# Kernel optimization log

Measured on AMD Instinct MI355X. Metric: run time of the kernel, lower is better.

Reference implementation:

```python
import jax, jax.numpy as jnp
import numpy as np

B, N, DIN, DOUT = 4, 4096, 128, 64
SCALE = float(DOUT)  # scale defaults to out_features


def setup_inputs() -> dict:
    key = jax.random.key(0)
    kx, kq, kk, kv = jax.random.split(key, 4)
    x = jax.random.normal(kx, (B, N, DIN), dtype=jnp.float32)
    # nn.Linear weights, stored as [in, out] so projection is x @ W
    Wq = jax.random.normal(kq, (DIN, DOUT), dtype=jnp.float32) * 0.02
    Wk = jax.random.normal(kk, (DIN, DOUT), dtype=jnp.float32) * 0.02
    Wv = jax.random.normal(kv, (DIN, DOUT), dtype=jnp.float32) * 0.02
    return {"x": x, "Wq": Wq, "Wk": Wk, "Wv": Wv}


def reference(x, Wq, Wk, Wv):
    # Projections: [B, N, DOUT]
    q = jnp.einsum("bnd,de->bne", x, Wq)
    k = jnp.einsum("bnd,de->bne", x, Wk)
    v = jnp.einsum("bnd,de->bne", x, Wv)
    # torch.cdist(q, k, p=2): Euclidean distance matrix [B, N, N]
    q_sq = jnp.sum(q * q, axis=-1)  # [B, N]
    k_sq = jnp.sum(k * k, axis=-1)  # [B, N]
    d2 = q_sq[:, :, None] + k_sq[:, None, :] - 2.0 * jnp.einsum("bne,bme->bnm", q, k)
    dist = jnp.sqrt(jnp.maximum(d2, 0.0))  # clamp for numerical safety
    att = jax.nn.softmax(dist / jnp.sqrt(jnp.float32(SCALE)), axis=-1)
    return jnp.einsum("bnm,bme->bne", att, v)
```

## Files before the change

kernel.cpp:

```cpp
#include <hip/hip_runtime.h>
#include <cstdint>
#include <cstddef>

#define B_ 4
#define N_ 4096
#define DIN_ 128

#define C2_ 0.0325213905f
#define NEG2C2_ (-0.0650427810f)

typedef __attribute__((ext_vector_type(8))) short short8;
typedef __attribute__((ext_vector_type(4))) float f32x4;
typedef __attribute__((ext_vector_type(4))) unsigned short us4;
typedef __attribute__((ext_vector_type(4))) unsigned int u32x4;

#if defined(__has_builtin)
#if __has_builtin(__builtin_amdgcn_exp2f)
#define EXP2(x) __builtin_amdgcn_exp2f(x)
#else
#define EXP2(x) exp2f(x)
#endif
#else
#define EXP2(x) exp2f(x)
#endif

__device__ __forceinline__ unsigned short f2bf(float f) {
    union { float f; unsigned int i; } v; v.f = f;
    unsigned int i = v.i;
    return (unsigned short)((i + 0x7FFFu + ((i >> 16) & 1u)) >> 16);
}

__device__ __forceinline__ unsigned int cvt_pk_bf16(float lo, float hi) {
    unsigned int r;
    asm("v_cvt_pk_bf16_f32 %0, %1, %2" : "=v"(r) : "v"(lo), "v"(hi));
    return r;
}

__global__ __launch_bounds__(256, 2) void proj_kernel(
    const float* __restrict__ x, const float* __restrict__ Wq,
    const float* __restrict__ Wk, const float* __restrict__ Wv,
    unsigned short* __restrict__ qb, unsigned short* __restrict__ kb,
    unsigned short* __restrict__ vT, float* __restrict__ qsq,
    float* __restrict__ ksq)
{
    __shared__ float xl[64 * 132];
    __shared__ float wl[128 * 64];
    const int t = threadIdx.x;
    const int R0 = blockIdx.x * 64;
    const int proj = blockIdx.y;
    const float* __restrict__ W = (proj == 0) ? Wq : ((proj == 1) ? Wk : Wv);

#pragma unroll
    for (int j = 0; j < 8; ++j) {
        const int i = t + 256 * j;
        const int row = i >> 5, dc = i & 31;
        *(float4*)(&xl[row * 132 + dc * 4]) =
            *(const float4*)(x + (size_t)(R0 + row) * DIN_ + dc * 4);
    }
#pragma unroll
    for (int j = 0; j < 8; ++j) {
        const int i = t + 256 * j;
        *(float4*)(&wl[i * 4]) = *(const float4*)(W + (size_t)i * 4);
    }
    __syncthreads();

    const int cg = t & 15, rg = t >> 4;
    const int c0 = cg * 4, r0 = rg * 4;

    float acc[4][4];
#pragma unroll
    for (int r = 0; r < 4; ++r)
#pragma unroll
        for (int c = 0; c < 4; ++c) acc[r][c] = 0.f;

    for (int d4 = 0; d4 < 32; ++d4) {
        float4 xv[4];
#pragma unroll
        for (int r = 0; r < 4; ++r)
            xv[r] = *(const float4*)(&xl[(r0 + r) * 132 + d4 * 4]);
#pragma unroll
        for (int dd = 0; dd < 4; ++dd) {
            const float4 wv = *(const float4*)(&wl[(d4 * 4 + dd) * 64 + c0]);
            const float wc[4] = { wv.x, wv.y, wv.z, wv.w };
#pragma unroll
            for (int r = 0; r < 4; ++r) {
                const float xr = ((const float*)&xv[r])[dd];
#pragma unroll
                for (int c = 0; c < 4; ++c)
                    acc[r][c] = fmaf(xr, wc[c], acc[r][c]);
            }
        }
    }

    if (proj < 2) {
        unsigned short* dst0 = (proj == 0) ? qb : kb;
#pragma unroll
        for (int r = 0; r < 4; ++r) {
            us4 pk = { f2bf(acc[r][0]), f2bf(acc[r][1]),
                       f2bf(acc[r][2]), f2bf(acc[r][3]) };
            *(us4*)(dst0 + (size_t)(R0 + r0 + r) * 64 + c0) = pk;
        }
#pragma unroll
        for (int r = 0; r < 4; ++r) {
            float s = 0.f;
#pragma unroll
            for (int c = 0; c < 4; ++c) s = fmaf(acc[r][c], acc[r][c], s);
            s += __shfl_xor(s, 1);
            s += __shfl_xor(s, 2);
            s += __shfl_xor(s, 4);
            s += __shfl_xor(s, 8);
            if (cg == 0) {
                float* sq = (proj == 0) ? qsq : ksq;
                sq[R0 + r0 + r] = s;
            }
        }
    } else {
        const int bb = R0 >> 12;
        const int n0 = (R0 & (N_ - 1)) + r0;
#pragma unroll
        for (int c = 0; c < 4; ++c) {
            us4 pk = { f2bf(acc[0][c]), f2bf(acc[1][c]),
                       f2bf(acc[2][c]), f2bf(acc[3][c]) };
            *(us4*)(vT + ((size_t)bb * 64 + (c0 + c)) * N_ + n0) = pk;
        }
    }
}

__global__ __launch_bounds__(256, 4) void attn_kernel(
    const unsigned short* __restrict__ qb, const unsigned short* __restrict__ kb,
    const unsigned short* __restrict__ vT, const float* __restrict__ qsq,
    const float* __restrict__ ksq, float* __restrict__ Opart,
    float* __restrict__ Lpart, int ktn)
{
    __shared__ __align__(16) char smem[8192 * 2 + 256];
    char* Klds = smem;
    char* Vlds = smem + 8192;
    float* ksql = (float*)(smem + 16384);

    const int t = threadIdx.x;
    const int w = t >> 6, lane = t & 63, li = lane & 15, g = lane >> 4;
    const int b = blockIdx.y, sp = blockIdx.z;
    const int q0 = blockIdx.x * 128;
    const int kt0 = sp * ktn;

    const size_t qbase = ((size_t)b * N_ + q0 + w * 32) * 64;
    short8 qa[2][2];
    float qsc[2];
#pragma unroll
    for (int h = 0; h < 2; ++h) {
        qa[h][0] = *(const short8*)(qb + qbase + (size_t)(h * 16 + li) * 64 + g * 8);
        qa[h][1] = *(const short8*)(qb + qbase + (size_t)(h * 16 + li) * 64 + 32 + g * 8);
        qsc[h] = qsq[(size_t)b * N_ + q0 + w * 32 + h * 16 + li] * C2_;
    }

    f32x4 oa[2][4];
    float lsum[2];
#pragma unroll
    for (int h = 0; h < 2; ++h) {
        lsum[h] = 0.f;
#pragma unroll
        for (int i = 0; i < 4; ++i) oa[h][i] = (f32x4){0.f, 0.f, 0.f, 0.f};
    }

    const unsigned short* kbb = kb + (size_t)b * N_ * 64;
    const unsigned short* vtb = vT + (size_t)b * 64 * N_;
    const float* ksqb = ksq + (size_t)b * N_;

    const int row0 = t >> 3, cc0 = t & 7;
    const int row1 = row0 + 32;
    const int lb0 = (row0 * 128 + cc0 * 16) ^ ((row0 & 7) << 4);
    const int lb1 = (row1 * 128 + cc0 * 16) ^ ((row1 & 7) << 4);

    const int krbase = ((li >> 2) << 3) + (li & 3);

    for (int ktl = 0; ktl < ktn; ++ktl) {
        const int kt = kt0 + ktl;
        *(uint4*)(Klds + lb0) = *(const uint4*)(kbb + (size_t)(kt * 64 + row0) * 64 + cc0 * 8);
        *(uint4*)(Klds + lb1) = *(const uint4*)(kbb + (size_t)(kt * 64 + row1) * 64 + cc0 * 8);
        *(uint4*)(Vlds + lb0) = *(const uint4*)(vtb + (size_t)row0 * N_ + kt * 64 + cc0 * 8);
        *(uint4*)(Vlds + lb1) = *(const uint4*)(vtb + (size_t)row1 * N_ + kt * 64 + cc0 * 8);
        if (t < 64) ksql[t] = ksqb[kt * 64 + t] * C2_;
        __syncthreads();

        u32x4 pa0[2], pa1[2];
#pragma unroll
        for (int c = 0; c < 4; ++c) {
            const int koff = ((c & 1) << 2) + ((c >> 1) << 5);
            const int kr = krbase + koff;
            const int sw = (kr & 7) << 4;
            const short8 kf0 = *(const short8*)(Klds + ((kr * 128 + g * 16) ^ sw));
            const short8 kf1 = *(const short8*)(Klds + ((kr * 128 + 64 + g * 16) ^ sw));
            f32x4 s[2];
            __builtin_amdgcn_s_setprio(1);
#pragma unroll
            for (int h = 0; h < 2; ++h) {
                s[h] = (f32x4){0.f, 0.f, 0.f, 0.f};
                s[h] = __builtin_amdgcn_mfma_f32_16x16x32_bf16(kf0, qa[h][0], s[h], 0, 0, 0);
                s[h] = __builtin_amdgcn_mfma_f32_16x16x32_bf16(kf1, qa[h][1], s[h], 0, 0, 0);
            }
            __builtin_amdgcn_s_setprio(0);

            const float4 ksc = *(const float4*)(ksql + 8 * g + koff);
            const float kscv[4] = { ksc.x, ksc.y, ksc.z, ksc.w };
#pragma unroll
            for (int h = 0; h < 2; ++h) {
                float p[4];
#pragma unroll
                for (int r = 0; r < 4; ++r) {
                    const float d2 = fmaf(NEG2C2_, s[h][r], qsc[h] + kscv[r]);
                    const float ds = __builtin_amdgcn_sqrtf(fmaxf(d2, 0.0f));
                    p[r] = EXP2(ds);
                    lsum[h] += p[r];
                }
                const unsigned int lo = cvt_pk_bf16(p[0], p[1]);
                const unsigned int hi = cvt_pk_bf16(p[2], p[3]);
                if (c == 0)      { pa0[h].x = lo; pa0[h].y = hi; }
                else if (c == 1) { pa0[h].z = lo; pa0[h].w = hi; }
                else if (c == 2) { pa1[h].x = lo; pa1[h].y = hi; }
                else             { pa1[h].z = lo; pa1[h].w = hi; }
            }
        }

        short8 paf[2][2];
#pragma unroll
        for (int h = 0; h < 2; ++h) {
            paf[h][0] = __builtin_bit_cast(short8, pa0[h]);
            paf[h][1] = __builtin_bit_cast(short8, pa1[h]);
        }
        __builtin_amdgcn_s_setprio(1);
#pragma unroll
        for (int c2 = 0; c2 < 4; ++c2) {
            const int er = c2 * 16 + li;
            const int swv = (er & 7) << 4;
            const short8 vf0 = *(const short8*)(Vlds + ((er * 128 + g * 16) ^ swv));
            const short8 vf1 = *(const short8*)(Vlds + ((er * 128 + 64 + g * 16) ^ swv));
#pragma unroll
            for (int h = 0; h < 2; ++h) {
                oa[h][c2] = __builtin_amdgcn_mfma_f32_16x16x32_bf16(paf[h][0], vf0, oa[h][c2], 0, 0, 0);
                oa[h][c2] = __builtin_amdgcn_mfma_f32_16x16x32_bf16(paf[h][1], vf1, oa[h][c2], 0, 0, 0);
            }
        }
        __builtin_amdgcn_s_setprio(0);
        __syncthreads();
    }

    const size_t obase = ((size_t)sp * B_ + b) * N_;
#pragma unroll
    for (int h = 0; h < 2; ++h) {
        float ls = lsum[h];
        ls += __shfl_xor(ls, 16);
        ls += __shfl_xor(ls, 32);
        if (lane < 16) Lpart[obase + q0 + w * 32 + h * 16 + li] = ls;
#pragma unroll
        for (int c2 = 0; c2 < 4; ++c2)
#pragma unroll
            for (int r = 0; r < 4; ++r)
                Opart[(obase + q0 + w * 32 + h * 16 + g * 4 + r) * 64 + c2 * 16 + li]
                    = oa[h][c2][r];
    }
}

__global__ __launch_bounds__(256) void reduce_kernel(
    const float* __restrict__ Opart, const float* __restrict__ Lpart,
    float* __restrict__ out, int S)
{
    const int idx = blockIdx.x * 256 + threadIdx.x;
    const int rowg = idx >> 4;
    const int e4 = (idx & 15) << 2;
    float l = 0.f;
    float4 o = {0.f, 0.f, 0.f, 0.f};
    for (int s = 0; s < S; ++s) {
        l += Lpart[(size_t)s * (B_ * N_) + rowg];
        const float4 v = *(const float4*)(Opart + ((size_t)s * (B_ * N_) + rowg) * 64 + e4);
        o.x += v.x; o.y += v.y; o.z += v.z; o.w += v.w;
    }
    const float inv = 1.0f / l;
    const float4 res = {o.x * inv, o.y * inv, o.z * inv, o.w * inv};
    *(float4*)(out + (size_t)rowg * 64 + e4) = res;
}

extern "C" void kernel_launch(void* const* d_in, const int* in_sizes, int n_in,
                              void* d_out, int out_size, void* d_ws, size_t ws_size,
                              hipStream_t stream) {
    (void)in_sizes; (void)n_in; (void)out_size;
    const float* x  = (const float*)d_in[0];
    const float* Wq = (const float*)d_in[1];
    const float* Wk = (const float*)d_in[2];
    const float* Wv = (const float*)d_in[3];

    char* ws = (char*)d_ws;
    const size_t MB = 1024 * 1024;
    unsigned short* qb = (unsigned short*)(ws);
    unsigned short* kb = (unsigned short*)(ws + 2 * MB);
    unsigned short* vT = (unsigned short*)(ws + 4 * MB);
    float* qsq = (float*)(ws + 6 * MB);
    float* ksq = (float*)(ws + 6 * MB + 65536);
    float* Lpart = (float*)(ws + 6 * MB + 262144);

    int S;
    float* Opart;
    if (ws_size >= 7 * MB + 32 * MB)      { S = 8; Opart = (float*)(ws + 7 * MB); }
    else if (ws_size >= 7 * MB + 16 * MB) { S = 4; Opart = (float*)(ws + 7 * MB); }
    else if (ws_size >= 7 * MB + 8 * MB)  { S = 2; Opart = (float*)(ws + 7 * MB); }
    else if (ws_size >= 7 * MB + 4 * MB)  { S = 1; Opart = (float*)(ws + 7 * MB); }
    else                                  { S = 1; Opart = (float*)d_out; }

    hipLaunchKernelGGL(proj_kernel, dim3(256, 3), dim3(256), 0, stream,
                       x, Wq, Wk, Wv, qb, kb, vT, qsq, ksq);
    hipLaunchKernelGGL(attn_kernel, dim3(32, B_, S), dim3(256), 0, stream,
                       qb, kb, vT, qsq, ksq, Opart, Lpart, 64 / S);
    hipLaunchKernelGGL(reduce_kernel, dim3(1024), dim3(256), 0, stream,
                       Opart, Lpart, (float*)d_out, S);
}
```

Before: 61.45 us.

## Compute QKV projection with bf16 MFMA in one fused block per row tile

The projection kernel converts x and the three weight matrices to bf16 in swizzled LDS and computes Q, K and V with 16x16x32 bf16 MFMA instructions instead of scalar fp32 FMAs. It also handles all three projections in a single block, so x is loaded once rather than three times, and the grid drops to 256 blocks. The cost is bf16 rounding of x and W before the matmul (a precision change), a larger LDS footprint, and scalar 2-byte stores for q and k.

```diff
diff --git a/kernel.cpp b/kernel.cpp
--- a/kernel.cpp
+++ b/kernel.cpp
@@ -43,85 +43,110 @@
     unsigned short* __restrict__ vT, float* __restrict__ qsq,
     float* __restrict__ ksq)
 {
-    __shared__ float xl[64 * 132];
-    __shared__ float wl[128 * 64];
+    __shared__ __align__(16) char smem[16384 + 3 * 16384];
+    char* xb = smem;
+
     const int t = threadIdx.x;
     const int R0 = blockIdx.x * 64;
-    const int proj = blockIdx.y;
-    const float* __restrict__ W = (proj == 0) ? Wq : ((proj == 1) ? Wk : Wv);
 
 #pragma unroll
     for (int j = 0; j < 8; ++j) {
         const int i = t + 256 * j;
-        const int row = i >> 5, dc = i & 31;
-        *(float4*)(&xl[row * 132 + dc * 4]) =
-            *(const float4*)(x + (size_t)(R0 + row) * DIN_ + dc * 4);
-    }
-#pragma unroll
-    for (int j = 0; j < 8; ++j) {
-        const int i = t + 256 * j;
-        *(float4*)(&wl[i * 4]) = *(const float4*)(W + (size_t)i * 4);
+        const int row = i >> 5, c4 = i & 31;
+        const float4 v = *(const float4*)(x + (size_t)(R0 + row) * DIN_ + c4 * 4);
+        uint2 p2;
+        p2.x = cvt_pk_bf16(v.x, v.y);
+        p2.y = cvt_pk_bf16(v.z, v.w);
+        *(uint2*)(xb + ((row * 256 + c4 * 8) ^ ((row & 7) << 4))) = p2;
+    }
+
+    {
+        const int c = t & 63, dg = t >> 6;
+        const int sw = (c & 7) << 4;
+#pragma unroll
+        for (int p = 0; p < 3; ++p) {
+            const float* __restrict__ Wp = (p == 0) ? Wq : ((p == 1) ? Wk : Wv);
+            char* wTp = smem + 16384 + p * 16384;
+            float wv[32];
+#pragma unroll
+            for (int d = 0; d < 32; ++d)
+                wv[d] = Wp[(size_t)(dg * 32 + d) * 64 + c];
+            unsigned int pk[16];
+#pragma unroll
+            for (int i = 0; i < 16; ++i) pk[i] = cvt_pk_bf16(wv[2 * i], wv[2 * i + 1]);
+#pragma unroll
+            for (int q16 = 0; q16 < 4; ++q16)
+                *(uint4*)(wTp + ((c * 256 + dg * 64 + q16 * 16) ^ sw)) =
+                    *(const uint4*)&pk[q16 * 4];
+        }
     }
     __syncthreads();
 
-    const int cg = t & 15, rg = t >> 4;
-    const int c0 = cg * 4, r0 = rg * 4;
-
-    float acc[4][4];
-#pragma unroll
-    for (int r = 0; r < 4; ++r)
-#pragma unroll
-        for (int c = 0; c < 4; ++c) acc[r][c] = 0.f;
-
-    for (int d4 = 0; d4 < 32; ++d4) {
-        float4 xv[4];
-#pragma unroll
-        for (int r = 0; r < 4; ++r)
-            xv[r] = *(const float4*)(&xl[(r0 + r) * 132 + d4 * 4]);
-#pragma unroll
-        for (int dd = 0; dd < 4; ++dd) {
-            const float4 wv = *(const float4*)(&wl[(d4 * 4 + dd) * 64 + c0]);
-            const float wc[4] = { wv.x, wv.y, wv.z, wv.w };
-#pragma unroll
-            for (int r = 0; r < 4; ++r) {
-                const float xr = ((const float*)&xv[r])[dd];
-#pragma unroll
-                for (int c = 0; c < 4; ++c)
-                    acc[r][c] = fmaf(xr, wc[c], acc[r][c]);
-            }
-        }
-    }
-
-    if (proj < 2) {
-        unsigned short* dst0 = (proj == 0) ? qb : kb;
-#pragma unroll
-        for (int r = 0; r < 4; ++r) {
-            us4 pk = { f2bf(acc[r][0]), f2bf(acc[r][1]),
-                       f2bf(acc[r][2]), f2bf(acc[r][3]) };
-            *(us4*)(dst0 + (size_t)(R0 + r0 + r) * 64 + c0) = pk;
-        }
+    const int w = t >> 6, lane = t & 63, li = lane & 15, g = lane >> 4;
+
+    short8 xa[4];
+    {
+        const int ar = w * 16 + li;
+        const int swa = (ar & 7) << 4;
+#pragma unroll
+        for (int s = 0; s < 4; ++s)
+            xa[s] = *(const short8*)(xb + ((ar * 256 + s * 64 + g * 16) ^ swa));
+    }
+
+    f32x4 acc[3][4];
+#pragma unroll
+    for (int p = 0; p < 3; ++p)
+#pragma unroll
+        for (int c2 = 0; c2 < 4; ++c2) acc[p][c2] = (f32x4){0.f, 0.f, 0.f, 0.f};
+
+#pragma unroll
+    for (int p = 0; p < 3; ++p) {
+        char* wTp = smem + 16384 + p * 16384;
+#pragma unroll
+        for (int c2 = 0; c2 < 4; ++c2) {
+            const int br = c2 * 16 + li;
+            const int swb = (br & 7) << 4;
+#pragma unroll
+            for (int s = 0; s < 4; ++s) {
+                const short8 wb = *(const short8*)(wTp + ((br * 256 + s * 64 + g * 16) ^ swb));
+                acc[p][c2] = __builtin_amdgcn_mfma_f32_16x16x32_bf16(xa[s], wb, acc[p][c2], 0, 0, 0);
+            }
+        }
+    }
+
+    const int rbase = R0 + w * 16 + g * 4;
+#pragma unroll
+    for (int p = 0; p < 2; ++p) {
+        unsigned short* dst = (p == 0) ? qb : kb;
+#pragma unroll
+        for (int c2 = 0; c2 < 4; ++c2)
+#pragma unroll
+            for (int r = 0; r < 4; ++r)
+                dst[(size_t)(rbase + r) * 64 + c2 * 16 + li] = f2bf(acc[p][c2][r]);
 #pragma unroll
         for (int r = 0; r < 4; ++r) {
             float s = 0.f;
 #pragma unroll
-            for (int c = 0; c < 4; ++c) s = fmaf(acc[r][c], acc[r][c], s);
+            for (int c2 = 0; c2 < 4; ++c2)
+                s = fmaf(acc[p][c2][r], acc[p][c2][r], s);
             s += __shfl_xor(s, 1);
             s += __shfl_xor(s, 2);
             s += __shfl_xor(s, 4);
             s += __shfl_xor(s, 8);
-            if (cg == 0) {
-                float* sq = (proj == 0) ? qsq : ksq;
-                sq[R0 + r0 + r] = s;
-            }
-        }
-    } else {
+            if (li == 0) {
+                float* sq = (p == 0) ? qsq : ksq;
+                sq[rbase + r] = s;
+            }
+        }
+    }
+    {
         const int bb = R0 >> 12;
-        const int n0 = (R0 & (N_ - 1)) + r0;
-#pragma unroll
-        for (int c = 0; c < 4; ++c) {
-            us4 pk = { f2bf(acc[0][c]), f2bf(acc[1][c]),
-                       f2bf(acc[2][c]), f2bf(acc[3][c]) };
-            *(us4*)(vT + ((size_t)bb * 64 + (c0 + c)) * N_ + n0) = pk;
+        const int n0 = (R0 & (N_ - 1)) + w * 16 + g * 4;
+#pragma unroll
+        for (int c2 = 0; c2 < 4; ++c2) {
+            us4 pk = { f2bf(acc[2][c2][0]), f2bf(acc[2][c2][1]),
+                       f2bf(acc[2][c2][2]), f2bf(acc[2][c2][3]) };
+            *(us4*)(vT + ((size_t)bb * 64 + c2 * 16 + li) * N_ + n0) = pk;
         }
     }
 }
@@ -305,7 +330,7 @@
     else if (ws_size >= 7 * MB + 4 * MB)  { S = 1; Opart = (float*)(ws + 7 * MB); }
     else                                  { S = 1; Opart = (float*)d_out; }
 
-    hipLaunchKernelGGL(proj_kernel, dim3(256, 3), dim3(256), 0, stream,
+    hipLaunchKernelGGL(proj_kernel, dim3(256), dim3(256), 0, stream,
                        x, Wq, Wk, Wv, qb, kb, vT, qsq, ksq);
     hipLaunchKernelGGL(attn_kernel, dim3(32, B_, S), dim3(256), 0, stream,
                        qb, kb, vT, qsq, ksq, Opart, Lpart, 64 / S);
```

Result: faster. 53.03 us (-13.7%).
